# Kernel optimization log

Hardware: AMD Instinct MI355X
Metric: run time of the kernel (lower is better)

Reference implementation:

```python
import jax, jax.numpy as jnp
import numpy as np

NUM_USERS = 200000
NUM_ITEMS = 100000
EMBED_DIM = 64
NUM_EDGES = 3200000


def setup_inputs() -> dict:
    key = jax.random.key(0)
    k1, k2, k3, k4, k5 = jax.random.split(key, 5)
    user_emb = jax.random.normal(k1, (NUM_USERS, EMBED_DIM), dtype=jnp.float32)
    item_emb = jax.random.normal(k2, (NUM_ITEMS, EMBED_DIM), dtype=jnp.float32)
    edge_user = jax.random.randint(k3, (NUM_EDGES,), 0, NUM_USERS, dtype=jnp.int32)
    edge_item = jax.random.randint(k4, (NUM_EDGES,), 0, NUM_ITEMS, dtype=jnp.int32)
    # normalized adjacency values (positive, like 1/sqrt(deg_u*deg_i))
    edge_val = jax.random.uniform(k5, (NUM_EDGES,), dtype=jnp.float32)
    return {
        "user_emb": user_emb,
        "item_emb": item_emb,
        "edge_user": edge_user,
        "edge_item": edge_item,
        "edge_val": edge_val,
    }


def reference(user_emb, item_emb, edge_user, edge_item, edge_val):
    # updated_users = ui_adj @ item_emb  (SpMM over COO edges)
    # gather item rows per edge, scale by adjacency value, scatter-add to users
    msg_to_users = edge_val[:, None] * item_emb[edge_item]  # [E, D]
    updated_users = jax.ops.segment_sum(msg_to_users, edge_user, num_segments=NUM_USERS)
    # updated_items = iu_adj @ user_emb  (iu_adj = ui_adj^T, same values)
    msg_to_items = edge_val[:, None] * user_emb[edge_user]  # [E, D]
    updated_items = jax.ops.segment_sum(msg_to_items, edge_item, num_segments=NUM_ITEMS)
    return updated_users, updated_items
```

## Files before the change

### kernel.cpp

```cpp
#include <hip/hip_runtime.h>

#define NU 200000
#define NI 100000
#define DIM 64
#define NE 3200000
#define NT (NU + NI)
#define CHUNK 2048
#define NB ((NT + CHUNK - 1) / CHUNK)

static_assert(NB <= 256, "scan2 assumes block sums fit one 256-thread block");


__device__ __forceinline__ int iclamp(int x, int lo, int hi) {
    return x < lo ? lo : (x > hi ? hi : x);
}

__global__ void zero_i32_kernel(int* __restrict__ p, long long n) {
    long long i = (long long)blockIdx.x * blockDim.x + threadIdx.x;
    long long stride = (long long)gridDim.x * blockDim.x;
    for (; i < n; i += stride) p[i] = 0;
}

__global__ void zero_f32_kernel(float* __restrict__ p, long long n) {
    long long i = (long long)blockIdx.x * blockDim.x + threadIdx.x;
    long long stride = (long long)gridDim.x * blockDim.x;
    for (; i < n; i += stride) p[i] = 0.0f;
}

__global__ void edge_detect_kernel(const int* __restrict__ a, const int* __restrict__ b,
                                   int n, int* __restrict__ flag) {
    int i = blockIdx.x * blockDim.x + threadIdx.x;
    int stride = gridDim.x * blockDim.x;
    int ma = 0, mb = 0;
    for (; i < n; i += stride) {
        ma = max(ma, a[i]);
        mb = max(mb, b[i]);
    }
    #pragma unroll
    for (int d = 32; d > 0; d >>= 1) {
        ma = max(ma, __shfl_down(ma, d, 64));
        mb = max(mb, __shfl_down(mb, d, 64));
    }
    if ((threadIdx.x & 63) == 0) {
        atomicMax(&flag[10], ma);
        atomicMax(&flag[11], mb);
    }
}
__global__ void finalize_kernel(int* __restrict__ flag) {
    if (threadIdx.x == 0 && blockIdx.x == 0) {
        int ma = flag[10], mb = flag[11];
        flag[3] = (mb >= NI && ma < NI) ? 1 : 0;
    }
}

__global__ __launch_bounds__(256) void hist_kernel(
        const int* __restrict__ a, const int* __restrict__ b,
        const int* __restrict__ flag, int* __restrict__ cnt) {
    int sw = flag[3];
    const int* eu = sw ? b : a;
    const int* ei = sw ? a : b;
    int e = blockIdx.x * blockDim.x + threadIdx.x;
    int stride = gridDim.x * blockDim.x;
    for (; e < NE; e += stride) {
        int u = iclamp(eu[e], 0, NU - 1);
        int i = iclamp(ei[e], 0, NI - 1);
        atomicAdd(&cnt[u], 1);
        atomicAdd(&cnt[NU + i], 1);
    }
}

__global__ __launch_bounds__(256) void scan1_kernel(const int* __restrict__ cnt,
                                                    int* __restrict__ bsum) {
    int b = blockIdx.x, t = threadIdx.x;
    int base = b * CHUNK;
    int sum = 0;
    #pragma unroll
    for (int k = 0; k < 8; ++k) {
        int idx = base + k * 256 + t;
        if (idx < NT) sum += cnt[idx];
    }
    #pragma unroll
    for (int d = 32; d > 0; d >>= 1) sum += __shfl_down(sum, d, 64);
    __shared__ int wsum[4];
    if ((t & 63) == 0) wsum[t >> 6] = sum;
    __syncthreads();
    if (t == 0) bsum[b] = wsum[0] + wsum[1] + wsum[2] + wsum[3];
}

__global__ __launch_bounds__(256) void scan2_kernel(int* __restrict__ bsum) {
    __shared__ int sh[256];
    int t = threadIdx.x;
    sh[t] = (t < NB) ? bsum[t] : 0;
    __syncthreads();
    for (int off = 1; off < 256; off <<= 1) {
        int v = (t >= off) ? sh[t - off] : 0;
        __syncthreads();
        sh[t] += v;
        __syncthreads();
    }
    if (t < NB) bsum[t] = (t == 0) ? 0 : sh[t - 1];
}

__global__ __launch_bounds__(256) void scan3_kernel(const int* __restrict__ cnt,
                                                    const int* __restrict__ bsum,
                                                    int* __restrict__ rowptr,
                                                    int* __restrict__ cursor) {
    int b = blockIdx.x, t = threadIdx.x;
    int base = b * CHUNK + t * 8;
    int v[8];
    int s = 0;
    #pragma unroll
    for (int k = 0; k < 8; ++k) {
        int idx = base + k;
        v[k] = (idx < NT) ? cnt[idx] : 0;
        s += v[k];
    }
    __shared__ int sh[256];
    sh[t] = s;
    __syncthreads();
    for (int off = 1; off < 256; off <<= 1) {
        int x = (t >= off) ? sh[t - off] : 0;
        __syncthreads();
        sh[t] += x;
        __syncthreads();
    }
    int run = (t == 0 ? 0 : sh[t - 1]) + bsum[b];
    #pragma unroll
    for (int k = 0; k < 8; ++k) {
        int idx = base + k;
        if (idx < NT) {
            rowptr[idx] = run;
            cursor[idx] = run;
            run += v[k];
        }
        if (idx == NT - 1) rowptr[NT] = run;
    }
}

__global__ __launch_bounds__(256) void scatter_kernel(
        const int* __restrict__ a, const int* __restrict__ b,
        const int* __restrict__ flag, const float* __restrict__ ev,
        int* __restrict__ cursor, int* __restrict__ colS, float* __restrict__ valS) {
    int sw = flag[3];
    const int* eu = sw ? b : a;
    const int* ei = sw ? a : b;
    int e = blockIdx.x * blockDim.x + threadIdx.x;
    int stride = gridDim.x * blockDim.x;
    for (; e < NE; e += stride) {
        int u = iclamp(eu[e], 0, NU - 1);
        int i = iclamp(ei[e], 0, NI - 1);
        float v = ev[e];
        int p0 = atomicAdd(&cursor[u], 1);
        colS[p0] = i; valS[p0] = v;
        int p1 = atomicAdd(&cursor[NU + i], 1);
        colS[p1] = u; valS[p1] = v;
    }
}

__global__ __launch_bounds__(256) void spmm_kernel(
        const int* __restrict__ rowptr, const int* __restrict__ colS,
        const float* __restrict__ valS, const float* __restrict__ emb,
        float* __restrict__ outp, int nrows, int row_off) {
    int gw = (int)(((long long)blockIdx.x * blockDim.x + threadIdx.x) >> 6);
    int lane = threadIdx.x & 63;
    if (gw >= nrows) return;
    int s = rowptr[row_off + gw];
    int e = rowptr[row_off + gw + 1];
    float acc0 = 0.0f, acc1 = 0.0f, acc2 = 0.0f, acc3 = 0.0f;
    int k = s;
    for (; k + 4 <= e; k += 4) {
        int c0 = colS[k];     float v0 = valS[k];
        int c1 = colS[k + 1]; float v1 = valS[k + 1];
        int c2 = colS[k + 2]; float v2 = valS[k + 2];
        int c3 = colS[k + 3]; float v3 = valS[k + 3];
        acc0 += v0 * emb[(size_t)c0 * DIM + lane];
        acc1 += v1 * emb[(size_t)c1 * DIM + lane];
        acc2 += v2 * emb[(size_t)c2 * DIM + lane];
        acc3 += v3 * emb[(size_t)c3 * DIM + lane];
    }
    for (; k < e; ++k) {
        int c = colS[k]; float v = valS[k];
        acc0 += v * emb[(size_t)c * DIM + lane];
    }
    outp[(size_t)gw * DIM + lane] = (acc0 + acc1) + (acc2 + acc3);
}

__global__ __launch_bounds__(256) void edge_atomic_kernel(
        const int* __restrict__ a, const int* __restrict__ b,
        const int* __restrict__ flag,
        const float* __restrict__ ev,
        const float* __restrict__ uemb, const float* __restrict__ iemb,
        float* __restrict__ outU, float* __restrict__ outI) {
    int sw = flag[3];
    const int* eu = sw ? b : a;
    const int* ei = sw ? a : b;
    long long t = (long long)blockIdx.x * blockDim.x + threadIdx.x;
    int lane = (int)(t & 63);
    long long e = t >> 6;
    if (e >= NE) return;
    int u = iclamp(eu[e], 0, NU - 1);
    int i = iclamp(ei[e], 0, NI - 1);
    float v  = ev[e];
    float xu = uemb[(size_t)u * DIM + lane];
    float xi = iemb[(size_t)i * DIM + lane];
    atomicAdd(&outU[(size_t)u * DIM + lane], v * xi);
    atomicAdd(&outI[(size_t)i * DIM + lane], v * xu);
}

extern "C" void kernel_launch(void* const* d_in, const int* in_sizes, int n_in,
                              void* d_out, int out_size, void* d_ws, size_t ws_size,
                              hipStream_t stream) {
    const float* user_emb = (const float*)d_in[0];
    const float* item_emb = (const float*)d_in[1];
    if (in_sizes[0] == NI * DIM && in_sizes[1] == NU * DIM) {
        user_emb = (const float*)d_in[1];
        item_emb = (const float*)d_in[0];
    }
    const int*   edge_a   = (const int*)d_in[2];
    const int*   edge_b   = (const int*)d_in[3];
    const float* edge_val = (const float*)d_in[4];

    float* out = (float*)d_out;
    float* out_users = out;
    float* out_items = out + (size_t)NU * DIM;

    const long long NOUT = (long long)(NU + NI) * DIM;

    int* flag = (int*)d_ws;
    const size_t need_units = (size_t)16 + NT + (NT + 1) + NT + 256
                            + (size_t)2 * NE + (size_t)2 * NE;
    const size_t need_bytes = need_units * 4;

    if (ws_size >= need_bytes) {
        int*   cnt    = flag + 16;
        int*   rowptr = cnt + NT;
        int*   cursor = rowptr + NT + 1;
        int*   bsum   = cursor + NT;
        int*   colS   = bsum + 256;
        float* valS   = (float*)(colS + (size_t)2 * NE);

        zero_i32_kernel<<<1024, 256, 0, stream>>>(flag, 16 + (long long)NT);
        edge_detect_kernel<<<512, 256, 0, stream>>>(edge_a, edge_b, NE, flag);
        finalize_kernel<<<1, 64, 0, stream>>>(flag);
        hist_kernel<<<3200, 256, 0, stream>>>(edge_a, edge_b, flag, cnt);
        scan1_kernel<<<NB, 256, 0, stream>>>(cnt, bsum);
        scan2_kernel<<<1, 256, 0, stream>>>(bsum);
        scan3_kernel<<<NB, 256, 0, stream>>>(cnt, bsum, rowptr, cursor);
        scatter_kernel<<<3200, 256, 0, stream>>>(edge_a, edge_b, flag, edge_val,
                                                 cursor, colS, valS);
        spmm_kernel<<<(NU * 64 + 255) / 256, 256, 0, stream>>>(
            rowptr, colS, valS, item_emb, out_users, NU, 0);
        spmm_kernel<<<(NI * 64 + 255) / 256, 256, 0, stream>>>(
            rowptr, colS, valS, user_emb, out_items, NI, NU);
    } else {
        zero_i32_kernel<<<1, 64, 0, stream>>>(flag, 16);
        edge_detect_kernel<<<512, 256, 0, stream>>>(edge_a, edge_b, NE, flag);
        finalize_kernel<<<1, 64, 0, stream>>>(flag);
        zero_f32_kernel<<<2048, 256, 0, stream>>>(out, NOUT);
        long long nthreads = (long long)NE * 64;
        edge_atomic_kernel<<<(int)(nthreads / 256), 256, 0, stream>>>(
            edge_a, edge_b, flag, edge_val, user_emb, item_emb, out_users, out_items);
    }
}
```

Measured before the change: 1.088 ms.

## Pack CSR column/value pairs and vectorize edge loads and SpMM gathers

Merges the separate column and value arrays into one interleaved int2 array, so each scatter writes one 8-byte entry and each SpMM step reads one. The histogram and scatter kernels load edges as int4/float4 with half the grid. The SpMM kernel splits each 64-lane wave into four 16-lane groups, each handling a different edge with float4 row loads, then combines the groups with xor shuffles. The aim is fewer memory transactions and more gathers in flight per row. The cost is extra shuffles and possible lane imbalance on short rows.

```diff
diff --git a/kernel.cpp b/kernel.cpp
--- a/kernel.cpp
+++ b/kernel.cpp
@@ -9,6 +9,7 @@
 #define NB ((NT + CHUNK - 1) / CHUNK)
 
 static_assert(NB <= 256, "scan2 assumes block sums fit one 256-thread block");
+static_assert((NE & 3) == 0, "int4 edge vectorization assumes NE % 4 == 0");
 
 
 __device__ __forceinline__ int iclamp(int x, int lo, int hi) {
@@ -57,15 +58,21 @@
         const int* __restrict__ a, const int* __restrict__ b,
         const int* __restrict__ flag, int* __restrict__ cnt) {
     int sw = flag[3];
-    const int* eu = sw ? b : a;
-    const int* ei = sw ? a : b;
-    int e = blockIdx.x * blockDim.x + threadIdx.x;
+    const int4* eu4 = (const int4*)(sw ? b : a);
+    const int4* ei4 = (const int4*)(sw ? a : b);
+    int e4 = blockIdx.x * blockDim.x + threadIdx.x;
     int stride = gridDim.x * blockDim.x;
-    for (; e < NE; e += stride) {
-        int u = iclamp(eu[e], 0, NU - 1);
-        int i = iclamp(ei[e], 0, NI - 1);
-        atomicAdd(&cnt[u], 1);
-        atomicAdd(&cnt[NU + i], 1);
+    for (; e4 < NE / 4; e4 += stride) {
+        int4 uu = eu4[e4];
+        int4 ii = ei4[e4];
+        atomicAdd(&cnt[iclamp(uu.x, 0, NU - 1)], 1);
+        atomicAdd(&cnt[iclamp(uu.y, 0, NU - 1)], 1);
+        atomicAdd(&cnt[iclamp(uu.z, 0, NU - 1)], 1);
+        atomicAdd(&cnt[iclamp(uu.w, 0, NU - 1)], 1);
+        atomicAdd(&cnt[NU + iclamp(ii.x, 0, NI - 1)], 1);
+        atomicAdd(&cnt[NU + iclamp(ii.y, 0, NI - 1)], 1);
+        atomicAdd(&cnt[NU + iclamp(ii.z, 0, NI - 1)], 1);
+        atomicAdd(&cnt[NU + iclamp(ii.w, 0, NI - 1)], 1);
     }
 }
 
@@ -140,49 +147,59 @@
 __global__ __launch_bounds__(256) void scatter_kernel(
         const int* __restrict__ a, const int* __restrict__ b,
         const int* __restrict__ flag, const float* __restrict__ ev,
-        int* __restrict__ cursor, int* __restrict__ colS, float* __restrict__ valS) {
+        int* __restrict__ cursor, int2* __restrict__ pairS) {
     int sw = flag[3];
-    const int* eu = sw ? b : a;
-    const int* ei = sw ? a : b;
-    int e = blockIdx.x * blockDim.x + threadIdx.x;
+    const int4* eu4 = (const int4*)(sw ? b : a);
+    const int4* ei4 = (const int4*)(sw ? a : b);
+    const float4* ev4 = (const float4*)ev;
+    int e4 = blockIdx.x * blockDim.x + threadIdx.x;
     int stride = gridDim.x * blockDim.x;
-    for (; e < NE; e += stride) {
-        int u = iclamp(eu[e], 0, NU - 1);
-        int i = iclamp(ei[e], 0, NI - 1);
-        float v = ev[e];
-        int p0 = atomicAdd(&cursor[u], 1);
-        colS[p0] = i; valS[p0] = v;
-        int p1 = atomicAdd(&cursor[NU + i], 1);
-        colS[p1] = u; valS[p1] = v;
+    for (; e4 < NE / 4; e4 += stride) {
+        int4 uu = eu4[e4];
+        int4 ii = ei4[e4];
+        float4 vv = ev4[e4];
+        int u[4] = {iclamp(uu.x,0,NU-1), iclamp(uu.y,0,NU-1),
+                    iclamp(uu.z,0,NU-1), iclamp(uu.w,0,NU-1)};
+        int i[4] = {iclamp(ii.x,0,NI-1), iclamp(ii.y,0,NI-1),
+                    iclamp(ii.z,0,NI-1), iclamp(ii.w,0,NI-1)};
+        float v[4] = {vv.x, vv.y, vv.z, vv.w};
+        #pragma unroll
+        for (int k = 0; k < 4; ++k) {
+            int p0 = atomicAdd(&cursor[u[k]], 1);
+            pairS[p0] = make_int2(i[k], __float_as_int(v[k]));
+            int p1 = atomicAdd(&cursor[NU + i[k]], 1);
+            pairS[p1] = make_int2(u[k], __float_as_int(v[k]));
+        }
     }
 }
 
 __global__ __launch_bounds__(256) void spmm_kernel(
-        const int* __restrict__ rowptr, const int* __restrict__ colS,
-        const float* __restrict__ valS, const float* __restrict__ emb,
+        const int* __restrict__ rowptr, const int2* __restrict__ pairS,
+        const float* __restrict__ emb,
         float* __restrict__ outp, int nrows, int row_off) {
     int gw = (int)(((long long)blockIdx.x * blockDim.x + threadIdx.x) >> 6);
     int lane = threadIdx.x & 63;
     if (gw >= nrows) return;
+    int g = lane >> 4;
+    int q = lane & 15;
     int s = rowptr[row_off + gw];
     int e = rowptr[row_off + gw + 1];
-    float acc0 = 0.0f, acc1 = 0.0f, acc2 = 0.0f, acc3 = 0.0f;
-    int k = s;
-    for (; k + 4 <= e; k += 4) {
-        int c0 = colS[k];     float v0 = valS[k];
-        int c1 = colS[k + 1]; float v1 = valS[k + 1];
-        int c2 = colS[k + 2]; float v2 = valS[k + 2];
-        int c3 = colS[k + 3]; float v3 = valS[k + 3];
-        acc0 += v0 * emb[(size_t)c0 * DIM + lane];
-        acc1 += v1 * emb[(size_t)c1 * DIM + lane];
-        acc2 += v2 * emb[(size_t)c2 * DIM + lane];
-        acc3 += v3 * emb[(size_t)c3 * DIM + lane];
-    }
-    for (; k < e; ++k) {
-        int c = colS[k]; float v = valS[k];
-        acc0 += v * emb[(size_t)c * DIM + lane];
-    }
-    outp[(size_t)gw * DIM + lane] = (acc0 + acc1) + (acc2 + acc3);
+    float ax = 0.0f, ay = 0.0f, az = 0.0f, aw = 0.0f;
+    for (int k = s + g; k < e; k += 4) {
+        int2 p = pairS[k];
+        float v = __int_as_float(p.y);
+        const float4* row = (const float4*)(emb + (size_t)p.x * DIM);
+        float4 x = row[q];
+        ax += v * x.x; ay += v * x.y; az += v * x.z; aw += v * x.w;
+    }
+    ax += __shfl_xor(ax, 16, 64); ay += __shfl_xor(ay, 16, 64);
+    az += __shfl_xor(az, 16, 64); aw += __shfl_xor(aw, 16, 64);
+    ax += __shfl_xor(ax, 32, 64); ay += __shfl_xor(ay, 32, 64);
+    az += __shfl_xor(az, 32, 64); aw += __shfl_xor(aw, 32, 64);
+    if (g == 0) {
+        float4* orow = (float4*)(outp + (size_t)gw * DIM);
+        orow[q] = make_float4(ax, ay, az, aw);
+    }
 }
 
 __global__ __launch_bounds__(256) void edge_atomic_kernel(
@@ -227,31 +244,30 @@
     const long long NOUT = (long long)(NU + NI) * DIM;
 
     int* flag = (int*)d_ws;
-    const size_t need_units = (size_t)16 + NT + (NT + 1) + NT + 256
-                            + (size_t)2 * NE + (size_t)2 * NE;
+    const size_t head_units = (size_t)16 + NT + (NT + 2) + NT + 256;
+    const size_t need_units = head_units + (size_t)4 * NE;
     const size_t need_bytes = need_units * 4;
 
     if (ws_size >= need_bytes) {
-        int*   cnt    = flag + 16;
-        int*   rowptr = cnt + NT;
-        int*   cursor = rowptr + NT + 1;
-        int*   bsum   = cursor + NT;
-        int*   colS   = bsum + 256;
-        float* valS   = (float*)(colS + (size_t)2 * NE);
+        int*  cnt    = flag + 16;
+        int*  rowptr = cnt + NT;
+        int*  cursor = rowptr + NT + 2;
+        int*  bsum   = cursor + NT;
+        int2* pairS  = (int2*)(bsum + 256);
 
         zero_i32_kernel<<<1024, 256, 0, stream>>>(flag, 16 + (long long)NT);
         edge_detect_kernel<<<512, 256, 0, stream>>>(edge_a, edge_b, NE, flag);
         finalize_kernel<<<1, 64, 0, stream>>>(flag);
-        hist_kernel<<<3200, 256, 0, stream>>>(edge_a, edge_b, flag, cnt);
+        hist_kernel<<<1600, 256, 0, stream>>>(edge_a, edge_b, flag, cnt);
         scan1_kernel<<<NB, 256, 0, stream>>>(cnt, bsum);
         scan2_kernel<<<1, 256, 0, stream>>>(bsum);
         scan3_kernel<<<NB, 256, 0, stream>>>(cnt, bsum, rowptr, cursor);
-        scatter_kernel<<<3200, 256, 0, stream>>>(edge_a, edge_b, flag, edge_val,
-                                                 cursor, colS, valS);
+        scatter_kernel<<<1600, 256, 0, stream>>>(edge_a, edge_b, flag, edge_val,
+                                                 cursor, pairS);
         spmm_kernel<<<(NU * 64 + 255) / 256, 256, 0, stream>>>(
-            rowptr, colS, valS, item_emb, out_users, NU, 0);
+            rowptr, pairS, item_emb, out_users, NU, 0);
         spmm_kernel<<<(NI * 64 + 255) / 256, 256, 0, stream>>>(
-            rowptr, colS, valS, user_emb, out_items, NI, NU);
+            rowptr, pairS, user_emb, out_items, NI, NU);
     } else {
         zero_i32_kernel<<<1, 64, 0, stream>>>(flag, 16);
         edge_detect_kernel<<<512, 256, 0, stream>>>(edge_a, edge_b, NE, flag);
```

Result: slower. 1.215 ms (+11.7%).
